# Optimization experiments

Hardware: AMD Instinct MI355X
Metric: run time of the kernel (lower is better)

The kernel has to match this reference:

```python
import jax, jax.numpy as jnp
import numpy as np

K = 4                 # max_block_size (depthwise conv kernel size)
BLOCKS = (1, 2, 3, 4) # block sizes, offset 0
DS = 4                # downsample_factor
BLOCK_MULT = 12       # lcm(1,2,3,4)
DIM = 512
NUM_TOKENS = 256


def setup_inputs() -> dict:
    key = jax.random.key(0)
    ks = jax.random.split(key, 8)
    b, n = 4, 4096
    s = 0.02
    return {
        "x": jax.random.randint(ks[0], (b, n), 0, NUM_TOKENS),
        "emb": jax.random.normal(ks[1], (NUM_TOKENS, DIM), dtype=jnp.float32) * s,
        "conv_w": jax.random.normal(ks[2], (DIM, K), dtype=jnp.float32) * s,   # depthwise Conv1d weight [d,1,K] squeezed
        "conv_b": jax.random.normal(ks[3], (DIM,), dtype=jnp.float32) * s,
        "proj_w": jax.random.normal(ks[4], (DIM, DIM), dtype=jnp.float32) * s,  # 1x1 conv == linear [out,in]
        "proj_b": jax.random.normal(ks[5], (DIM,), dtype=jnp.float32) * s,
        "score_w": jax.random.normal(ks[6], (DIM,), dtype=jnp.float32) * s,     # nn.Linear(dim,1)
        "score_b": jax.random.normal(ks[7], (), dtype=jnp.float32) * s,
    }


def reference(x, emb, conv_w, conv_b, proj_w, proj_b, score_w, score_b):
    b, n = x.shape
    h = emb[x]  # [b, n, d] token embedding (gather)

    # pos_conv: pad (K-1) at sequence end, depthwise conv (valid), then pointwise proj
    hp = jnp.pad(h, ((0, 0), (0, K - 1), (0, 0)))
    y = conv_b + sum(hp[:, k:k + n, :] * conv_w[:, k] for k in range(K))  # [b, n, d]
    h = y @ proj_w.T + proj_b

    # pad sequence to multiple of lcm of block sizes
    L = -(-n // BLOCK_MULT) * BLOCK_MULT
    h = jnp.pad(h, ((0, 0), (0, L - n), (0, 0)))

    # multi-scale block mean pooling, upsampled back to length L
    reprs = []
    for bs in BLOCKS:
        r = h.reshape(b, L // bs, bs, DIM).mean(axis=2)     # [b, L/bs, d]
        reprs.append(jnp.repeat(r, bs, axis=1))             # [b, L, d]
    block_reprs = jnp.stack(reprs, axis=2)                  # [b, L, nb, d]

    # per-position block scores
    scores = block_reprs @ score_w + score_b                # [b, L, nb]
    scores = jax.nn.softmax(scores, axis=2)

    # consensus attention over positions (d = nb = len(BLOCKS))
    sim = jnp.einsum('bid,bjd->bij', scores, scores)        # [b, L, L]
    attn = jax.nn.softmax(sim, axis=-1)
    scores = jnp.einsum('bij,bjm->bim', attn, scores)       # [b, L, nb]

    # fuse block representations and downsample
    out = jnp.einsum('bnkd,bnk->bnd', block_reprs, scores)  # [b, L, d]
    m = -(-n // DS) * DS                                    # == n (4096 divisible by 4)
    out = out[:, :m].reshape(b, m // DS, DS, DIM).mean(axis=2)
    return out
```

## Files before the change

### kernel.cpp

```cpp
#include <hip/hip_runtime.h>
#include <hip/hip_bf16.h>

#define B_ 4
#define N_ 4096
#define L_ 4104
#define D_ 512
#define CH2 129
#define BK 64
#define NF 210

typedef __attribute__((ext_vector_type(8))) short bf16x8;
typedef __attribute__((ext_vector_type(4))) float f32x4;

__device__ __forceinline__ float bf2f(unsigned short u) {
  union { unsigned u; float f; } c; c.u = ((unsigned)u) << 16; return c.f;
}

__global__ __launch_bounds__(256) void k_g(const float* __restrict__ emb,
    const float* __restrict__ pw, const float* __restrict__ cwp,
    const float* __restrict__ cb, const float* __restrict__ pb,
    float* __restrict__ G, float* __restrict__ biasp,
    unsigned* __restrict__ featPk, float* __restrict__ featCf) {
  __shared__ __align__(16) __hip_bfloat16 As[2][64 * BK];
  __shared__ __align__(16) __hip_bfloat16 Bs[2][128 * BK];
  __shared__ __align__(16) float cwS[512];
  __shared__ float red[4];
  const int bx = blockIdx.x;
  const int t = threadIdx.x;
  const int w = t >> 6, l = t & 63;

  if (bx == 128) {
    if (t < NF) {
      int idx = 0, mp = 0, mq = 0, mr = 0, ms = 0;
      for (int m = 0; m <= 6; ++m)
        for (int p = m; p >= 0; --p)
          for (int q = m - p; q >= 0; --q)
            for (int r = m - p - q; r >= 0; --r) {
              const int s4 = m - p - q - r;
              if (idx == t) { mp = p; mq = q; mr = r; ms = s4; }
              ++idx;
            }
      featPk[t] = (unsigned)mp | ((unsigned)mq << 8) | ((unsigned)mr << 16) | ((unsigned)ms << 24);
      const float invf[7] = {1.f, 1.f, 0.5f, 1.f/6.f, 1.f/24.f, 1.f/120.f, 1.f/720.f};
      featCf[t] = invf[mp] * invf[mq] * invf[mr] * invf[ms];
    }
    return;
  }
  if (bx >= 64) {
    const int o0 = (bx - 64) * 8;
    const float2 cv = *(const float2*)(cb + t * 2);
#pragma unroll
    for (int oo = 0; oo < 8; ++oo) {
      const int o = o0 + oo;
      const float2 wv = *(const float2*)(pw + (size_t)o * 512 + t * 2);
      float s = wv.x * cv.x + wv.y * cv.y;
#pragma unroll
      for (int off = 32; off > 0; off >>= 1) s += __shfl_xor(s, off);
      if (l == 0) red[w] = s;
      __syncthreads();
      if (t == 0) biasp[o] = red[0] + red[1] + red[2] + red[3] + pb[o];
      __syncthreads();
    }
    return;
  }

  const int m0 = (bx & 3) * 64;
  const int n0 = ((bx >> 2) & 3) * 128;
  const int kp = bx >> 4;
  const int quad = l >> 4, r16 = l & 15;
  const int wc = w * 32;

  cwS[t]       = cwp[t * 4 + kp];
  cwS[t + 256] = cwp[(t + 256) * 4 + kp];

  f32x4 acc[4][2];
#pragma unroll
  for (int a = 0; a < 4; ++a)
#pragma unroll
    for (int bq = 0; bq < 2; ++bq) acc[a][bq] = (f32x4){0.f, 0.f, 0.f, 0.f};

  const int ra = t >> 2, ga0 = (t & 3) * 2;
  const int rb = t >> 1, gb0 = (t & 1) * 4;

#define STAGEG(buf, kb)                                                          \
  _Pragma("unroll")                                                              \
  for (int gi = 0; gi < 2; ++gi) {                                               \
    const int g = ga0 + gi;                                                      \
    const int c0 = (kb) + g * 8;                                                 \
    const float4 a0 = *(const float4*)(emb + (size_t)(m0 + ra) * 512 + c0);      \
    const float4 a1 = *(const float4*)(emb + (size_t)(m0 + ra) * 512 + c0 + 4);  \
    const float4 w0 = *(const float4*)(cwS + c0);                                \
    const float4 w1 = *(const float4*)(cwS + c0 + 4);                            \
    union { __hip_bfloat16 q[8]; bf16x8 v; } ua;                                 \
    ua.q[0] = __float2bfloat16(a0.x * w0.x); ua.q[1] = __float2bfloat16(a0.y * w0.y); \
    ua.q[2] = __float2bfloat16(a0.z * w0.z); ua.q[3] = __float2bfloat16(a0.w * w0.w); \
    ua.q[4] = __float2bfloat16(a1.x * w1.x); ua.q[5] = __float2bfloat16(a1.y * w1.y); \
    ua.q[6] = __float2bfloat16(a1.z * w1.z); ua.q[7] = __float2bfloat16(a1.w * w1.w); \
    *(bf16x8*)(&As[buf][ra * BK + ((g ^ (ra & 7)) * 8)]) = ua.v;                 \
  }                                                                              \
  _Pragma("unroll")                                                              \
  for (int gi = 0; gi < 4; ++gi) {                                               \
    const int g = gb0 + gi;                                                      \
    const int c0 = (kb) + g * 8;                                                 \
    const float4 b0 = *(const float4*)(pw + (size_t)(n0 + rb) * 512 + c0);       \
    const float4 b1 = *(const float4*)(pw + (size_t)(n0 + rb) * 512 + c0 + 4);   \
    union { __hip_bfloat16 q[8]; bf16x8 v; } ub;                                 \
    ub.q[0] = __float2bfloat16(b0.x); ub.q[1] = __float2bfloat16(b0.y);          \
    ub.q[2] = __float2bfloat16(b0.z); ub.q[3] = __float2bfloat16(b0.w);          \
    ub.q[4] = __float2bfloat16(b1.x); ub.q[5] = __float2bfloat16(b1.y);          \
    ub.q[6] = __float2bfloat16(b1.z); ub.q[7] = __float2bfloat16(b1.w);          \
    *(bf16x8*)(&Bs[buf][rb * BK + ((g ^ (rb & 7)) * 8)]) = ub.v;                 \
  }

  __syncthreads();
  STAGEG(0, 0)
  __syncthreads();

#pragma unroll 1
  for (int kt = 0; kt < 8; ++kt) {
    const int cur = kt & 1;
    if (kt < 7) { STAGEG(1 - cur, (kt + 1) * BK) }
#pragma unroll
    for (int kk = 0; kk < 2; ++kk) {
      const int col_e = (kk * 32 + quad * 8) ^ ((r16 & 7) * 8);
      bf16x8 af[4], bfr[2];
#pragma unroll
      for (int ti = 0; ti < 4; ++ti)
        af[ti] = *(const bf16x8*)(&As[cur][(ti * 16 + r16) * BK + col_e]);
#pragma unroll
      for (int tj = 0; tj < 2; ++tj)
        bfr[tj] = *(const bf16x8*)(&Bs[cur][(wc + tj * 16 + r16) * BK + col_e]);
#pragma unroll
      for (int ti = 0; ti < 4; ++ti)
#pragma unroll
        for (int tj = 0; tj < 2; ++tj)
          acc[ti][tj] = __builtin_amdgcn_mfma_f32_16x16x32_bf16(af[ti], bfr[tj], acc[ti][tj], 0, 0, 0);
    }
    __syncthreads();
  }
#undef STAGEG

#pragma unroll
  for (int ti = 0; ti < 4; ++ti) {
    const int gi0 = m0 + ti * 16 + quad * 4;
#pragma unroll
    for (int tj = 0; tj < 2; ++tj) {
      const int go = n0 + wc + tj * 16 + r16;
#pragma unroll
      for (int r = 0; r < 4; ++r)
        G[((size_t)kp * 256 + gi0 + r) * 512 + go] = acc[ti][tj][r];
    }
  }
}

__global__ __launch_bounds__(256) void k_h(const int* __restrict__ x,
    const float* __restrict__ G, const float* __restrict__ biasp,
    const float* __restrict__ sw, unsigned* __restrict__ h,
    float* __restrict__ tb, float* __restrict__ Zg) {
  __shared__ int tokS[11];
  __shared__ float tpart[8][4];
  const int bx = blockIdx.x;
  const int b = bx >> 9, i0 = (bx & 511) * 8;
  const int t = threadIdx.x, d = t * 2, w = t >> 6, l = t & 63;
  if (bx < 17) {
    const int zi = bx * 256 + t;
    if (zi < B_ * NF * 5) Zg[zi] = 0.f;
  }
  if (t < 11) {
    const int j = i0 + t;
    tokS[t] = (j < N_) ? x[b * N_ + j] : 0;
  }
  __syncthreads();
  const float2 bp  = *(const float2*)(biasp + d);
  const float2 swv = *(const float2*)(sw + d);
#pragma unroll
  for (int r = 0; r < 8; ++r) {
    const int i = i0 + r;
    float2 acc = bp;
#pragma unroll
    for (int k = 0; k < 4; ++k) {
      if (i + k < N_) {
        const float2 g = *(const float2*)(G + ((size_t)k * 256 + tokS[r + k]) * 512 + d);
        acc.x += g.x; acc.y += g.y;
      }
    }
    union { __hip_bfloat16 q[2]; unsigned u; } pk;
    pk.q[0] = __float2bfloat16(acc.x);
    pk.q[1] = __float2bfloat16(acc.y);
    h[(size_t)(b * N_ + i) * 256 + t] = pk.u;
    float v = acc.x * swv.x + acc.y * swv.y;
#pragma unroll
    for (int off = 32; off > 0; off >>= 1) v += __shfl_xor(v, off);
    if (l == 0) tpart[r][w] = v;
  }
  __syncthreads();
  if (t < 8)
    tb[b * N_ + i0 + t] = tpart[t][0] + tpart[t][1] + tpart[t][2] + tpart[t][3];
}

__device__ __forceinline__ float4 softmax4(const float* __restrict__ tw, int base,
                                           int i, float bb) {
  const float s0 = tw[i - base] + bb;
  const int j2 = i & ~1;
  const float s1 = (tw[j2 - base] + tw[j2 + 1 - base]) * 0.5f + bb;
  const int j3 = (i / 3) * 3;
  const float s2 = (tw[j3 - base] + tw[j3 + 1 - base] + tw[j3 + 2 - base]) * (1.f / 3.f) + bb;
  const int j4 = i & ~3;
  const float s3 = (tw[j4 - base] + tw[j4 + 1 - base] + tw[j4 + 2 - base] + tw[j4 + 3 - base]) * 0.25f + bb;
  const float m = fmaxf(fmaxf(s0, s1), fmaxf(s2, s3));
  const float e0 = __expf(s0 - m), e1 = __expf(s1 - m), e2 = __expf(s2 - m), e3 = __expf(s3 - m);
  const float inv = 1.f / (e0 + e1 + e2 + e3);
  return make_float4(e0 * inv, e1 * inv, e2 * inv, e3 * inv);
}

__global__ __launch_bounds__(256) void k_zphi(const float* __restrict__ tb,
    const float* __restrict__ sb, const unsigned* __restrict__ featPk,
    const float* __restrict__ featCf, float* __restrict__ Zg) {
  __shared__ float twj[135];
  __shared__ float P[CH2][32];
  __shared__ unsigned pkS[NF];
  const int bx = blockIdx.x;
  const int b = bx >> 5, jc = bx & 31;
  const int t = threadIdx.x;
  const int j0 = jc * CH2;
  const int rowb = b * N_;
  const int len = min(CH2, L_ - j0);
  if (t < NF) pkS[t] = featPk[t];
  for (int idx = t; idx < 135; idx += 256) {
    const int j = j0 - 3 + idx;
    twj[idx] = (j >= 0 && j < N_) ? tb[rowb + j] : 0.f;
  }
  __syncthreads();
  const float bb = sb[0];
  if (t < len) {
    const float4 s = softmax4(twj, j0 - 3, j0 + t, bb);
    float* p = &P[t][0];
    float va = 1.f, vb = 1.f, vc = 1.f, vd = 1.f;
    p[0] = 1.f; p[8] = 1.f; p[16] = 1.f; p[24] = 1.f;
#pragma unroll
    for (int e = 1; e < 8; ++e) {
      va *= s.x; vb *= s.y; vc *= s.z; vd *= s.w;
      p[e] = va; p[8 + e] = vb; p[16 + e] = vc; p[24 + e] = vd;
    }
  }
  __syncthreads();
  if (t < NF) {
    const unsigned pk = pkS[t];
    const int p = pk & 255, q = (pk >> 8) & 255, r = (pk >> 16) & 255, s4 = pk >> 24;
    float z0 = 0.f, z1 = 0.f, z2 = 0.f, z3 = 0.f, z4 = 0.f;
    for (int jj = 0; jj < len; ++jj) {
      const float* pp = &P[jj][0];
      const float pa0 = pp[p],       pa1 = pp[p + 1];
      const float pb0 = pp[8 + q],   pb1 = pp[8 + q + 1];
      const float pc0 = pp[16 + r],  pc1 = pp[16 + r + 1];
      const float pd0 = pp[24 + s4], pd1 = pp[24 + s4 + 1];
      const float cd = pc0 * pd0, ab = pa0 * pb0;
      z4 += pa0 * (pb0 * cd);
      z0 += pa1 * (pb0 * cd);
      z1 += pb1 * (pa0 * cd);
      z2 += pc1 * (ab * pd0);
      z3 += pd1 * (ab * pc0);
    }
    float* zb = Zg + (size_t)(b * NF + t) * 5;
    atomicAdd(zb + 0, z0); atomicAdd(zb + 1, z1); atomicAdd(zb + 2, z2);
    atomicAdd(zb + 3, z3); atomicAdd(zb + 4, z4);
  }
}

__global__ __launch_bounds__(256) void k_fuse(const __hip_bfloat16* __restrict__ h,
    const float* __restrict__ tb, const float* __restrict__ sb,
    const unsigned* __restrict__ featPk, const float* __restrict__ featCf,
    const float* __restrict__ Zg, float* __restrict__ out) {
  __shared__ __align__(16) float4 wgtS[12];
  __shared__ float tbS[12];
  __shared__ float Pr[12][32];
  __shared__ float Zl[NF * 5];
  __shared__ unsigned pkS[NF];
  __shared__ float cfS[NF];
  const int bx = blockIdx.x;
  const int b = bx / 342, j12 = bx % 342;
  const int t = threadIdx.x, d = t * 2;
  const int r0 = 12 * j12;

  if (t < NF) { pkS[t] = featPk[t]; cfS[t] = featCf[t]; }
  for (int i2 = t; i2 < NF * 5; i2 += 256) Zl[i2] = Zg[(size_t)b * NF * 5 + i2];
  if (t < 12) {
    const int row = r0 + t;
    tbS[t] = (row < N_) ? tb[b * N_ + row] : 0.f;
  }
  __syncthreads();
  if (t < 12) {
    const float4 s = softmax4(tbS, r0, r0 + t, sb[0]);
    float* p = &Pr[t][0];
    float va = 1.f, vb = 1.f, vc = 1.f, vd = 1.f;
    p[0] = 1.f; p[8] = 1.f; p[16] = 1.f; p[24] = 1.f;
#pragma unroll
    for (int e = 1; e < 8; ++e) {
      va *= s.x; vb *= s.y; vc *= s.z; vd *= s.w;
      p[e] = va; p[8 + e] = vb; p[16 + e] = vc; p[24 + e] = vd;
    }
  }
  __syncthreads();
  if (t < 192) {
    const int row = t >> 4, fi = t & 15;
    float n0 = 0.f, n1 = 0.f, n2 = 0.f, n3 = 0.f, dn = 0.f;
    const float* pr = &Pr[row][0];
    for (int f = fi; f < NF; f += 16) {
      const unsigned pk = pkS[f];
      const float val = cfS[f] * pr[pk & 255] * pr[8 + ((pk >> 8) & 255)]
                                * pr[16 + ((pk >> 16) & 255)] * pr[24 + (pk >> 24)];
      const float* z = &Zl[f * 5];
      n0 += val * z[0]; n1 += val * z[1]; n2 += val * z[2]; n3 += val * z[3];
      dn += val * z[4];
    }
#pragma unroll
    for (int m = 8; m >= 1; m >>= 1) {
      n0 += __shfl_xor(n0, m); n1 += __shfl_xor(n1, m); n2 += __shfl_xor(n2, m);
      n3 += __shfl_xor(n3, m); dn += __shfl_xor(dn, m);
    }
    if (fi == 0) {
      const float inv = 1.f / dn;
      wgtS[row] = make_float4(n0 * inv, n1 * inv, n2 * inv, n3 * inv);
    }
  }
  __syncthreads();

  const __hip_bfloat16* hb = h + (size_t)b * N_ * D_;
  float2 hv[12];
#pragma unroll
  for (int q = 0; q < 12; ++q) {
    const int row = r0 + q;
    if (row < N_) {
      const ushort2 u = *(const ushort2*)(hb + (size_t)row * D_ + d);
      hv[q] = make_float2(bf2f(u.x), bf2f(u.y));
    } else {
      hv[q] = make_float2(0.f, 0.f);
    }
  }

  float2 p2[6], p3[4], p4[3];
#pragma unroll
  for (int g = 0; g < 6; ++g) {
    p2[g].x = (hv[2 * g].x + hv[2 * g + 1].x) * 0.5f;
    p2[g].y = (hv[2 * g].y + hv[2 * g + 1].y) * 0.5f;
  }
#pragma unroll
  for (int g = 0; g < 4; ++g) {
    p3[g].x = (hv[3 * g].x + hv[3 * g + 1].x + hv[3 * g + 2].x) * (1.f / 3.f);
    p3[g].y = (hv[3 * g].y + hv[3 * g + 1].y + hv[3 * g + 2].y) * (1.f / 3.f);
  }
#pragma unroll
  for (int g = 0; g < 3; ++g) {
    p4[g].x = (hv[4 * g].x + hv[4 * g + 1].x + hv[4 * g + 2].x + hv[4 * g + 3].x) * 0.25f;
    p4[g].y = (hv[4 * g].y + hv[4 * g + 1].y + hv[4 * g + 2].y + hv[4 * g + 3].y) * 0.25f;
  }

#pragma unroll
  for (int o = 0; o < 3; ++o) {
    const int orow = j12 * 3 + o;
    if (orow < 1024) {
      float ox = 0.f, oy = 0.f;
#pragma unroll
      for (int rr = 0; rr < 4; ++rr) {
        const int r = 4 * o + rr;
        const float4 wv = wgtS[r];
        const float2 p1 = hv[r];
        const float2 q2 = p2[r >> 1];
        const float2 q3 = p3[r / 3];
        const float2 q4 = p4[o];
        ox += wv.x * p1.x + wv.y * q2.x + wv.z * q3.x + wv.w * q4.x;
        oy += wv.x * p1.y + wv.y * q2.y + wv.z * q3.y + wv.w * q4.y;
      }
      float2 ov; ov.x = ox * 0.25f; ov.y = oy * 0.25f;
      *(float2*)(out + (size_t)(b * 1024 + orow) * D_ + d) = ov;
    }
  }
}

extern "C" void kernel_launch(void* const* d_in, const int* in_sizes, int n_in,
                              void* d_out, int out_size, void* d_ws, size_t ws_size,
                              hipStream_t stream) {
  const int*   x       = (const int*)d_in[0];
  const float* emb     = (const float*)d_in[1];
  const float* conv_w  = (const float*)d_in[2];
  const float* conv_b  = (const float*)d_in[3];
  const float* proj_w  = (const float*)d_in[4];
  const float* proj_b  = (const float*)d_in[5];
  const float* score_w = (const float*)d_in[6];
  const float* score_b = (const float*)d_in[7];
  float* out = (float*)d_out;

  char* ws = (char*)d_ws;
  size_t off = 0;
  float*          G    = (float*)(ws + off);          off += (size_t)4 * 256 * 512 * 4;
  float*          bias = (float*)(ws + off);          off += (size_t)512 * 4;
  __hip_bfloat16* h    = (__hip_bfloat16*)(ws + off); off += (size_t)16384 * 512 * 2;
  float*          tb   = (float*)(ws + off);          off += (size_t)16384 * 4;
  float*          Zg   = (float*)(ws + off);          off += (size_t)B_ * NF * 5 * 4;
  unsigned*       featPk = (unsigned*)(ws + off);     off += (size_t)NF * 4;
  float*          featCf = (float*)(ws + off);        off += (size_t)NF * 4;
  (void)in_sizes; (void)n_in; (void)out_size; (void)ws_size;

  k_g<<<129, 256, 0, stream>>>(emb, proj_w, conv_w, conv_b, proj_b, G, bias, featPk, featCf);
  k_h<<<2048, 256, 0, stream>>>(x, G, bias, score_w, (unsigned*)h, tb, Zg);
  k_zphi<<<B_ * 32, 256, 0, stream>>>(tb, score_b, featPk, featCf, Zg);
  k_fuse<<<B_ * 342, 256, 0, stream>>>(h, tb, score_b, featPk, featCf, Zg, out);
}
```

Before: 127.2 us.

## Eliminate h materialization by precomputing per-token score tables and recomputing h in fuse

Removes the k_h kernel that wrote a bf16 h tensor and per-position score dots. k_g gains four extra blocks that fold the score vector through proj_w and the conv taps into per-token score tables (TS) plus a constant, so scores become four table lookups. k_fuse rebuilds h rows directly from G via token gathers instead of reading h, and k_zphi is re-chunked into smaller chunks with more blocks. This drops one launch and a large intermediate write/read, at the cost of redundant gathers of G and a serial matvec in the new k_g blocks.

```diff
diff --git a/kernel.cpp b/kernel.cpp
--- a/kernel.cpp
+++ b/kernel.cpp
@@ -5,31 +5,79 @@
 #define N_ 4096
 #define L_ 4104
 #define D_ 512
-#define CH2 129
 #define BK 64
 #define NF 210
+#define ZCH 36
+#define ZCHUNKS 114
 
 typedef __attribute__((ext_vector_type(8))) short bf16x8;
 typedef __attribute__((ext_vector_type(4))) float f32x4;
-
-__device__ __forceinline__ float bf2f(unsigned short u) {
-  union { unsigned u; float f; } c; c.u = ((unsigned)u) << 16; return c.f;
-}
 
 __global__ __launch_bounds__(256) void k_g(const float* __restrict__ emb,
     const float* __restrict__ pw, const float* __restrict__ cwp,
     const float* __restrict__ cb, const float* __restrict__ pb,
+    const float* __restrict__ sw,
     float* __restrict__ G, float* __restrict__ biasp,
-    unsigned* __restrict__ featPk, float* __restrict__ featCf) {
+    unsigned* __restrict__ featPk, float* __restrict__ featCf,
+    float* __restrict__ Zg, float* __restrict__ TS, float* __restrict__ c0g) {
   __shared__ __align__(16) __hip_bfloat16 As[2][64 * BK];
   __shared__ __align__(16) __hip_bfloat16 Bs[2][128 * BK];
   __shared__ __align__(16) float cwS[512];
   __shared__ float red[4];
+  __shared__ __align__(16) float swS[512];
+  __shared__ __align__(16) float uS[512];
+  __shared__ __align__(16) float vkS[512];
   const int bx = blockIdx.x;
   const int t = threadIdx.x;
   const int w = t >> 6, l = t & 63;
 
+  if (bx >= 129) {
+    const int kp = bx - 129;
+    swS[t] = sw[t]; swS[t + 256] = sw[t + 256];
+    __syncthreads();
+    const int c2 = t * 2;
+    float ux0 = 0.f, uy0 = 0.f, ux1 = 0.f, uy1 = 0.f;
+#pragma unroll 4
+    for (int o = 0; o < 512; o += 2) {
+      const float s0 = swS[o], s1 = swS[o + 1];
+      const float2 w0 = *(const float2*)(pw + (size_t)o * 512 + c2);
+      const float2 w1 = *(const float2*)(pw + (size_t)(o + 1) * 512 + c2);
+      ux0 += s0 * w0.x; uy0 += s0 * w0.y;
+      ux1 += s1 * w1.x; uy1 += s1 * w1.y;
+    }
+    const float ux = ux0 + ux1, uy = uy0 + uy1;
+    uS[c2] = ux; uS[c2 + 1] = uy;
+    vkS[c2]     = ux * cwp[c2 * 4 + kp];
+    vkS[c2 + 1] = uy * cwp[(c2 + 1) * 4 + kp];
+    __syncthreads();
+    const int r16 = t & 15, tg = t >> 4;
+    for (int tok0 = 0; tok0 < 256; tok0 += 16) {
+      const int tok = tok0 + tg;
+      float dot = 0.f;
+#pragma unroll
+      for (int it = 0; it < 8; ++it) {
+        const int c = it * 64 + r16 * 4;
+        const float4 e4 = *(const float4*)(emb + (size_t)tok * 512 + c);
+        const float4 v4 = *(const float4*)(vkS + c);
+        dot += e4.x * v4.x + e4.y * v4.y + e4.z * v4.z + e4.w * v4.w;
+      }
+#pragma unroll
+      for (int m = 8; m >= 1; m >>= 1) dot += __shfl_xor(dot, m);
+      if (r16 == 0) TS[kp * 256 + tok] = dot;
+    }
+    if (kp == 0) {
+      float part = cb[c2] * uS[c2] + cb[c2 + 1] * uS[c2 + 1]
+                 + pb[c2] * swS[c2] + pb[c2 + 1] * swS[c2 + 1];
+#pragma unroll
+      for (int m = 32; m >= 1; m >>= 1) part += __shfl_xor(part, m);
+      if (l == 0) red[w] = part;
+      __syncthreads();
+      if (t == 0) c0g[0] = red[0] + red[1] + red[2] + red[3];
+    }
+    return;
+  }
   if (bx == 128) {
+    for (int zi = t; zi < B_ * NF * 5; zi += 256) Zg[zi] = 0.f;
     if (t < NF) {
       int idx = 0, mp = 0, mq = 0, mr = 0, ms = 0;
       for (int m = 0; m <= 6; ++m)
@@ -153,51 +201,6 @@
   }
 }
 
-__global__ __launch_bounds__(256) void k_h(const int* __restrict__ x,
-    const float* __restrict__ G, const float* __restrict__ biasp,
-    const float* __restrict__ sw, unsigned* __restrict__ h,
-    float* __restrict__ tb, float* __restrict__ Zg) {
-  __shared__ int tokS[11];
-  __shared__ float tpart[8][4];
-  const int bx = blockIdx.x;
-  const int b = bx >> 9, i0 = (bx & 511) * 8;
-  const int t = threadIdx.x, d = t * 2, w = t >> 6, l = t & 63;
-  if (bx < 17) {
-    const int zi = bx * 256 + t;
-    if (zi < B_ * NF * 5) Zg[zi] = 0.f;
-  }
-  if (t < 11) {
-    const int j = i0 + t;
-    tokS[t] = (j < N_) ? x[b * N_ + j] : 0;
-  }
-  __syncthreads();
-  const float2 bp  = *(const float2*)(biasp + d);
-  const float2 swv = *(const float2*)(sw + d);
-#pragma unroll
-  for (int r = 0; r < 8; ++r) {
-    const int i = i0 + r;
-    float2 acc = bp;
-#pragma unroll
-    for (int k = 0; k < 4; ++k) {
-      if (i + k < N_) {
-        const float2 g = *(const float2*)(G + ((size_t)k * 256 + tokS[r + k]) * 512 + d);
-        acc.x += g.x; acc.y += g.y;
-      }
-    }
-    union { __hip_bfloat16 q[2]; unsigned u; } pk;
-    pk.q[0] = __float2bfloat16(acc.x);
-    pk.q[1] = __float2bfloat16(acc.y);
-    h[(size_t)(b * N_ + i) * 256 + t] = pk.u;
-    float v = acc.x * swv.x + acc.y * swv.y;
-#pragma unroll
-    for (int off = 32; off > 0; off >>= 1) v += __shfl_xor(v, off);
-    if (l == 0) tpart[r][w] = v;
-  }
-  __syncthreads();
-  if (t < 8)
-    tb[b * N_ + i0 + t] = tpart[t][0] + tpart[t][1] + tpart[t][2] + tpart[t][3];
-}
-
 __device__ __forceinline__ float4 softmax4(const float* __restrict__ tw, int base,
                                            int i, float bb) {
   const float s0 = tw[i - base] + bb;
@@ -213,27 +216,34 @@
   return make_float4(e0 * inv, e1 * inv, e2 * inv, e3 * inv);
 }
 
-__global__ __launch_bounds__(256) void k_zphi(const float* __restrict__ tb,
+__global__ __launch_bounds__(256) void k_zphi(const int* __restrict__ x,
+    const float* __restrict__ TS, const float* __restrict__ c0g,
     const float* __restrict__ sb, const unsigned* __restrict__ featPk,
-    const float* __restrict__ featCf, float* __restrict__ Zg) {
-  __shared__ float twj[135];
-  __shared__ float P[CH2][32];
+    float* __restrict__ Zg) {
+  __shared__ float twj[ZCH];
+  __shared__ float P[ZCH][32];
   __shared__ unsigned pkS[NF];
   const int bx = blockIdx.x;
-  const int b = bx >> 5, jc = bx & 31;
+  const int b = bx / ZCHUNKS, jc = bx % ZCHUNKS;
   const int t = threadIdx.x;
-  const int j0 = jc * CH2;
-  const int rowb = b * N_;
-  const int len = min(CH2, L_ - j0);
+  const int j0 = jc * ZCH;
   if (t < NF) pkS[t] = featPk[t];
-  for (int idx = t; idx < 135; idx += 256) {
-    const int j = j0 - 3 + idx;
-    twj[idx] = (j >= 0 && j < N_) ? tb[rowb + j] : 0.f;
+  if (t < ZCH) {
+    const int j = j0 + t;
+    float tv = 0.f;
+    if (j < N_) {
+      tv = c0g[0];
+      const int* xb = x + b * N_;
+#pragma unroll
+      for (int k = 0; k < 4; ++k)
+        if (j + k < N_) tv += TS[k * 256 + xb[j + k]];
+    }
+    twj[t] = tv;
   }
   __syncthreads();
   const float bb = sb[0];
-  if (t < len) {
-    const float4 s = softmax4(twj, j0 - 3, j0 + t, bb);
+  if (t < ZCH) {
+    const float4 s = softmax4(twj, j0, j0 + t, bb);
     float* p = &P[t][0];
     float va = 1.f, vb = 1.f, vc = 1.f, vd = 1.f;
     p[0] = 1.f; p[8] = 1.f; p[16] = 1.f; p[24] = 1.f;
@@ -248,7 +258,8 @@
     const unsigned pk = pkS[t];
     const int p = pk & 255, q = (pk >> 8) & 255, r = (pk >> 16) & 255, s4 = pk >> 24;
     float z0 = 0.f, z1 = 0.f, z2 = 0.f, z3 = 0.f, z4 = 0.f;
-    for (int jj = 0; jj < len; ++jj) {
+#pragma unroll 2
+    for (int jj = 0; jj < ZCH; ++jj) {
       const float* pp = &P[jj][0];
       const float pa0 = pp[p],       pa1 = pp[p + 1];
       const float pb0 = pp[8 + q],   pb1 = pp[8 + q + 1];
@@ -267,16 +278,19 @@
   }
 }
 
-__global__ __launch_bounds__(256) void k_fuse(const __hip_bfloat16* __restrict__ h,
-    const float* __restrict__ tb, const float* __restrict__ sb,
-    const unsigned* __restrict__ featPk, const float* __restrict__ featCf,
-    const float* __restrict__ Zg, float* __restrict__ out) {
+__global__ __launch_bounds__(256) void k_fuse(const int* __restrict__ x,
+    const float* __restrict__ G, const float* __restrict__ biasp,
+    const float* __restrict__ TS, const float* __restrict__ c0g,
+    const float* __restrict__ sb, const unsigned* __restrict__ featPk,
+    const float* __restrict__ featCf, const float* __restrict__ Zg,
+    float* __restrict__ out) {
   __shared__ __align__(16) float4 wgtS[12];
   __shared__ float tbS[12];
   __shared__ float Pr[12][32];
   __shared__ float Zl[NF * 5];
   __shared__ unsigned pkS[NF];
   __shared__ float cfS[NF];
+  __shared__ int tokS[16];
   const int bx = blockIdx.x;
   const int b = bx / 342, j12 = bx % 342;
   const int t = threadIdx.x, d = t * 2;
@@ -284,9 +298,43 @@
 
   if (t < NF) { pkS[t] = featPk[t]; cfS[t] = featCf[t]; }
   for (int i2 = t; i2 < NF * 5; i2 += 256) Zl[i2] = Zg[(size_t)b * NF * 5 + i2];
+  if (t < 15) {
+    const int j = r0 + t;
+    tokS[t] = (j < N_) ? x[b * N_ + j] : -1;
+  }
+  __syncthreads();
+
+  const float2 bp = *(const float2*)(biasp + d);
+  float2 hv[12];
+#pragma unroll
+  for (int q = 0; q < 12; ++q) {
+    float2 a = make_float2(0.f, 0.f);
+    if (r0 + q < N_) {
+      a = bp;
+#pragma unroll
+      for (int k = 0; k < 4; ++k) {
+        const int tk = tokS[q + k];
+        if (tk >= 0) {
+          const float2 g = *(const float2*)(G + ((size_t)k * 256 + tk) * 512 + d);
+          a.x += g.x; a.y += g.y;
+        }
+      }
+    }
+    hv[q] = a;
+  }
+
   if (t < 12) {
     const int row = r0 + t;
-    tbS[t] = (row < N_) ? tb[b * N_ + row] : 0.f;
+    float tv = 0.f;
+    if (row < N_) {
+      tv = c0g[0];
+#pragma unroll
+      for (int k = 0; k < 4; ++k) {
+        const int tk = tokS[t + k];
+        if (tk >= 0) tv += TS[k * 256 + tk];
+      }
+    }
+    tbS[t] = tv;
   }
   __syncthreads();
   if (t < 12) {
@@ -324,19 +372,6 @@
     }
   }
   __syncthreads();
-
-  const __hip_bfloat16* hb = h + (size_t)b * N_ * D_;
-  float2 hv[12];
-#pragma unroll
-  for (int q = 0; q < 12; ++q) {
-    const int row = r0 + q;
-    if (row < N_) {
-      const ushort2 u = *(const ushort2*)(hb + (size_t)row * D_ + d);
-      hv[q] = make_float2(bf2f(u.x), bf2f(u.y));
-    } else {
-      hv[q] = make_float2(0.f, 0.f);
-    }
-  }
 
   float2 p2[6], p3[4], p4[3];
 #pragma unroll
@@ -392,17 +427,17 @@
 
   char* ws = (char*)d_ws;
   size_t off = 0;
-  float*          G    = (float*)(ws + off);          off += (size_t)4 * 256 * 512 * 4;
-  float*          bias = (float*)(ws + off);          off += (size_t)512 * 4;
-  __hip_bfloat16* h    = (__hip_bfloat16*)(ws + off); off += (size_t)16384 * 512 * 2;
-  float*          tb   = (float*)(ws + off);          off += (size_t)16384 * 4;
-  float*          Zg   = (float*)(ws + off);          off += (size_t)B_ * NF * 5 * 4;
-  unsigned*       featPk = (unsigned*)(ws + off);     off += (size_t)NF * 4;
-  float*          featCf = (float*)(ws + off);        off += (size_t)NF * 4;
+  float*    G      = (float*)(ws + off); off += (size_t)4 * 256 * 512 * 4;
+  float*    bias   = (float*)(ws + off); off += (size_t)512 * 4;
+  float*    Zg     = (float*)(ws + off); off += (size_t)B_ * NF * 5 * 4;
+  unsigned* featPk = (unsigned*)(ws + off); off += (size_t)1024;
+  float*    featCf = (float*)(ws + off); off += (size_t)1024;
+  float*    TS     = (float*)(ws + off); off += (size_t)4 * 256 * 4;
+  float*    c0     = (float*)(ws + off); off += (size_t)16;
   (void)in_sizes; (void)n_in; (void)out_size; (void)ws_size;
 
-  k_g<<<129, 256, 0, stream>>>(emb, proj_w, conv_w, conv_b, proj_b, G, bias, featPk, featCf);
-  k_h<<<2048, 256, 0, stream>>>(x, G, bias, score_w, (unsigned*)h, tb, Zg);
-  k_zphi<<<B_ * 32, 256, 0, stream>>>(tb, score_b, featPk, featCf, Zg);
-  k_fuse<<<B_ * 342, 256, 0, stream>>>(h, tb, score_b, featPk, featCf, Zg, out);
+  k_g<<<133, 256, 0, stream>>>(emb, proj_w, conv_w, conv_b, proj_b, score_w,
+                               G, bias, featPk, featCf, Zg, TS, c0);
+  k_zphi<<<B_ * ZCHUNKS, 256, 0, stream>>>(x, TS, c0, score_b, featPk, Zg);
+  k_fuse<<<B_ * 342, 256, 0, stream>>>(x, G, bias, TS, c0, score_b, featPk, featCf, Zg, out);
 }
```

New measurement: 150.0 us. +18.0%, slower.
